# Kernel optimization log

Measured on AMD Instinct MI355X. Metric: run time of the kernel, lower is better.

The kernel has to match this reference:

```python
import jax, jax.numpy as jnp
import numpy as np

N = 6144
F_IN, H1, H2, EMB = 512, 256, 128, 64
ALPHA = 0.2  # LeakyReLU negative slope
NEG_INF = -9e15


def setup_inputs() -> dict:
    key = jax.random.key(0)
    ks = jax.random.split(key, 12)
    x = jax.random.normal(ks[0], (N, F_IN), dtype=jnp.float32)
    adj = (jax.random.uniform(ks[1], (N, N)) < 0.01).astype(jnp.float32)
    adj = jnp.maximum(adj, jnp.eye(N, dtype=jnp.float32))
    M = jax.random.uniform(ks[2], (N, N), dtype=jnp.float32)

    def glorot(k, shape):
        lim = float(np.sqrt(6.0 / (shape[0] + shape[1])))
        return jax.random.uniform(k, shape, jnp.float32, -lim, lim)

    params = {
        "W1": glorot(ks[3], (F_IN, H1)), "a_s1": glorot(ks[4], (H1, 1)), "a_n1": glorot(ks[5], (H1, 1)),
        "W2": glorot(ks[6], (H1, H2)),  "a_s2": glorot(ks[7], (H2, 1)), "a_n2": glorot(ks[8], (H2, 1)),
        "W3": glorot(ks[9], (H2, EMB)), "a_s3": glorot(ks[10], (EMB, 1)), "a_n3": glorot(ks[11], (EMB, 1)),
    }
    return {"x": x, "adj": adj, "M": M, **params}


def _gat_layer(x, adj, M, W, a_s, a_n):
    h = x @ W                                   # [N, d_out]
    e = (h @ a_s) + (h @ a_n).T                 # [N, N] pairwise logits
    e = jax.nn.leaky_relu(e * M, ALPHA)
    e = jnp.where(adj > 0, e, NEG_INF)
    att = jax.nn.softmax(e, axis=1)             # masked row softmax
    return jax.nn.elu(att @ h)


def reference(x, adj, M, W1, a_s1, a_n1, W2, a_s2, a_n2, W3, a_s3, a_n3):
    h = _gat_layer(x, adj, M, W1, a_s1, a_n1)
    h = _gat_layer(h, adj, M, W2, a_s2, a_n2)
    h = _gat_layer(h, adj, M, W3, a_s3, a_n3)
    z = h / jnp.maximum(jnp.linalg.norm(h, axis=1, keepdims=True), 1e-12)
    A_pred = jax.nn.sigmoid(z @ z.T)
    return (A_pred, z)
```

## Files before the change

### kernel.cpp

```cpp
#include <hip/hip_runtime.h>
#include <hip/hip_bf16.h>
#include <math.h>

#define NROW 6144
#define LRELU_ALPHA 0.2f
#define MAXD 128

typedef __attribute__((ext_vector_type(8))) __bf16 bf16x8;
typedef __attribute__((ext_vector_type(16))) float f32x16;

__global__ __launch_bounds__(256) void prep_all(
    const float* __restrict__ adj, const float* __restrict__ Mm,
    int* __restrict__ cnt, int* __restrict__ cidx, float* __restrict__ cmval,
    const float* __restrict__ W1, const float* __restrict__ W2, const float* __restrict__ W3,
    __bf16* __restrict__ w1h, __bf16* __restrict__ w1l,
    __bf16* __restrict__ w2h, __bf16* __restrict__ w2l,
    __bf16* __restrict__ w3h, __bf16* __restrict__ w3l,
    const float* __restrict__ as1, const float* __restrict__ an1,
    const float* __restrict__ as2, const float* __restrict__ an2,
    const float* __restrict__ as3, const float* __restrict__ an3,
    float* __restrict__ wsa1, float* __restrict__ wna1,
    float* __restrict__ wsa2, float* __restrict__ wna2,
    float* __restrict__ wsa3, float* __restrict__ wna3) {
  int b = blockIdx.x;
  if (b < NROW) {
    const int row = b;
    const int wv = threadIdx.x >> 6, lane = threadIdx.x & 63;
    __shared__ int wcnt[4];
    __shared__ int js[MAXD];
    const float4* arow = (const float4*)(adj + (size_t)row * NROW);
    const float* mrow = Mm + (size_t)row * NROW;
    float4 a[6];
#pragma unroll
    for (int it = 0; it < 6; ++it) a[it] = arow[wv * 384 + it * 64 + lane];
    int pc = 0;
#pragma unroll
    for (int it = 0; it < 6; ++it)
      pc += (a[it].x > 0.f) + (a[it].y > 0.f) + (a[it].z > 0.f) + (a[it].w > 0.f);
#pragma unroll
    for (int off = 32; off; off >>= 1) pc += __shfl_xor(pc, off);
    if (lane == 0) wcnt[wv] = pc;
    __syncthreads();
    int base = 0;
    for (int w = 0; w < wv; ++w) base += wcnt[w];
    const int total = min(wcnt[0] + wcnt[1] + wcnt[2] + wcnt[3], MAXD);
    const unsigned long long lmask = (1ull << lane) - 1ull;
#pragma unroll
    for (int it = 0; it < 6; ++it) {
      const int j = wv * 1536 + it * 256 + lane * 4;
      unsigned long long m;
      m = __ballot(a[it].x > 0.f);
      if (a[it].x > 0.f) { int p = base + __popcll(m & lmask); if (p < MAXD) js[p] = j; }
      base += __popcll(m);
      m = __ballot(a[it].y > 0.f);
      if (a[it].y > 0.f) { int p = base + __popcll(m & lmask); if (p < MAXD) js[p] = j + 1; }
      base += __popcll(m);
      m = __ballot(a[it].z > 0.f);
      if (a[it].z > 0.f) { int p = base + __popcll(m & lmask); if (p < MAXD) js[p] = j + 2; }
      base += __popcll(m);
      m = __ballot(a[it].w > 0.f);
      if (a[it].w > 0.f) { int p = base + __popcll(m & lmask); if (p < MAXD) js[p] = j + 3; }
      base += __popcll(m);
    }
    __syncthreads();
    for (int k = threadIdx.x; k < total; k += 256) {
      int j = js[k];
      cidx[(size_t)row * MAXD + k] = j;
      cmval[(size_t)row * MAXD + k] = mrow[j];
    }
    if (threadIdx.x == 0) cnt[row] = total;
    return;
  }
  b -= NROW;
  if (b < 672) {
    int idx = b * 256 + threadIdx.x;
    const float* W; __bf16 *wh, *wl; int K, D;
    if (idx < 131072) { W = W1; wh = w1h; wl = w1l; K = 512; D = 256; }
    else if (idx < 163840) { idx -= 131072; W = W2; wh = w2h; wl = w2l; K = 256; D = 128; }
    else { idx -= 163840; if (idx >= 8192) return; W = W3; wh = w3h; wl = w3l; K = 128; D = 64; }
    int k = idx / D, d = idx - k * D;
    float v = W[idx];
    __bf16 h = (__bf16)v;
    wh[(size_t)d * K + k] = h;
    wl[(size_t)d * K + k] = (__bf16)(v - (float)h);
    return;
  }
  b -= 672;
  int t = b * 256 + threadIdx.x;
  if (t < 512) {
    float s = 0.f, n = 0.f;
    for (int d = 0; d < 256; ++d) { float w = W1[t * 256 + d]; s = fmaf(w, as1[d], s); n = fmaf(w, an1[d], n); }
    wsa1[t] = s; wna1[t] = n;
  } else if (t < 768) {
    int k = t - 512;
    float s = 0.f, n = 0.f;
    for (int d = 0; d < 128; ++d) { float w = W2[k * 128 + d]; s = fmaf(w, as2[d], s); n = fmaf(w, an2[d], n); }
    wsa2[k] = s; wna2[k] = n;
  } else if (t < 896) {
    int k = t - 768;
    float s = 0.f, n = 0.f;
    for (int d = 0; d < 64; ++d) { float w = W3[k * 64 + d]; s = fmaf(w, as3[d], s); n = fmaf(w, an3[d], n); }
    wsa3[k] = s; wna3[k] = n;
  }
}

__global__ __launch_bounds__(256) void gemm_mfma(const float* __restrict__ A,
                                                 const __bf16* __restrict__ Bth,
                                                 const __bf16* __restrict__ Btl,
                                                 const float* __restrict__ wsa,
                                                 const float* __restrict__ wna,
                                                 float* __restrict__ sv,
                                                 float* __restrict__ nv,
                                                 float* __restrict__ C,
                                                 __bf16* __restrict__ Cb, int K, int D) {
  const int wv = threadIdx.x >> 6, lane = threadIdx.x & 63;
  const int l31 = lane & 31, lh = lane >> 5;
  const int ib = blockIdx.x * 64 + (wv >> 1) * 32;
  const int jb = blockIdx.y * 64 + (wv & 1) * 32;
  const float* Arow = A + (size_t)(ib + l31) * K + lh * 8;
  const __bf16* Bh = Bth + (size_t)(jb + l31) * K + lh * 8;
  const __bf16* Bl = Btl + (size_t)(jb + l31) * K + lh * 8;
  const bool do_sn = (blockIdx.y == 0) && ((wv & 1) == 0);
  f32x16 acc;
#pragma unroll
  for (int r = 0; r < 16; ++r) acc[r] = 0.f;
  float ss = 0.f, nn = 0.f;
  for (int k = 0; k < K; k += 16) {
    float4 a0 = *(const float4*)(Arow + k);
    float4 a1 = *(const float4*)(Arow + k + 4);
    bf16x8 bh = *(const bf16x8*)(Bh + k);
    bf16x8 bl = *(const bf16x8*)(Bl + k);
    float av[8] = {a0.x, a0.y, a0.z, a0.w, a1.x, a1.y, a1.z, a1.w};
    if (do_sn) {
      float4 s0 = *(const float4*)(wsa + k + lh * 8);
      float4 s1 = *(const float4*)(wsa + k + lh * 8 + 4);
      float4 n0 = *(const float4*)(wna + k + lh * 8);
      float4 n1 = *(const float4*)(wna + k + lh * 8 + 4);
      ss = fmaf(av[0], s0.x, ss); ss = fmaf(av[1], s0.y, ss);
      ss = fmaf(av[2], s0.z, ss); ss = fmaf(av[3], s0.w, ss);
      ss = fmaf(av[4], s1.x, ss); ss = fmaf(av[5], s1.y, ss);
      ss = fmaf(av[6], s1.z, ss); ss = fmaf(av[7], s1.w, ss);
      nn = fmaf(av[0], n0.x, nn); nn = fmaf(av[1], n0.y, nn);
      nn = fmaf(av[2], n0.z, nn); nn = fmaf(av[3], n0.w, nn);
      nn = fmaf(av[4], n1.x, nn); nn = fmaf(av[5], n1.y, nn);
      nn = fmaf(av[6], n1.z, nn); nn = fmaf(av[7], n1.w, nn);
    }
    bf16x8 ah, al;
#pragma unroll
    for (int t = 0; t < 8; ++t) {
      __bf16 h = (__bf16)av[t];
      ah[t] = h;
      al[t] = (__bf16)(av[t] - (float)h);
    }
    acc = __builtin_amdgcn_mfma_f32_32x32x16_bf16(ah, bh, acc, 0, 0, 0);
    acc = __builtin_amdgcn_mfma_f32_32x32x16_bf16(ah, bl, acc, 0, 0, 0);
    acc = __builtin_amdgcn_mfma_f32_32x32x16_bf16(al, bh, acc, 0, 0, 0);
  }
  if (do_sn) {
    ss += __shfl_xor(ss, 32);
    nn += __shfl_xor(nn, 32);
    if (lh == 0) { sv[ib + l31] = ss; nv[ib + l31] = nn; }
  }
#pragma unroll
  for (int r = 0; r < 16; ++r) {
    int rowi = (r & 3) + 8 * (r >> 2) + 4 * lh;
    C[(size_t)(ib + rowi) * D + jb + l31] = acc[r];
    if (Cb) Cb[(size_t)(ib + rowi) * D + jb + l31] = (__bf16)acc[r];
  }
}

template <int D, int WPR, bool BF16G, bool NORM>
__global__ __launch_bounds__(256) void attn_csr(const float* __restrict__ h,
                                                const __bf16* __restrict__ hb,
                                                const int* __restrict__ cnt,
                                                const int* __restrict__ cidx,
                                                const float* __restrict__ cmval,
                                                const float* __restrict__ sv,
                                                const float* __restrict__ nv,
                                                float* __restrict__ out,
                                                __bf16* __restrict__ zb) {
  constexpr int RPB = 4 / WPR;
  constexpr int CW = D / WPR;
  constexpr int NQ = BF16G ? 2 : CW / 64;
  __shared__ float ws[4][MAXD];
  __shared__ int js[4][MAXD];
  const int wv = threadIdx.x >> 6, lane = threadIdx.x & 63;
  const int row = blockIdx.x * RPB + wv / WPR;
  const int half = wv % WPR;
  const int c = cnt[row];
  const float si = sv[row];
  const size_t cb = (size_t)row * MAXD;

  float e0 = -1e30f, e1 = -1e30f;
  int j0 = 0, j1 = 0;
  if (lane < c) {
    j0 = cidx[cb + lane];
    float v = (si + nv[j0]) * cmval[cb + lane];
    e0 = v > 0.f ? v : LRELU_ALPHA * v;
  }
  if (lane + 64 < c) {
    j1 = cidx[cb + lane + 64];
    float v = (si + nv[j1]) * cmval[cb + lane + 64];
    e1 = v > 0.f ? v : LRELU_ALPHA * v;
  }
  float mx = fmaxf(e0, e1);
#pragma unroll
  for (int off = 32; off; off >>= 1) mx = fmaxf(mx, __shfl_xor(mx, off));
  float w0 = lane < c ? __expf(e0 - mx) : 0.f;
  float w1 = lane + 64 < c ? __expf(e1 - mx) : 0.f;
  float s = w0 + w1;
#pragma unroll
  for (int off = 32; off; off >>= 1) s += __shfl_xor(s, off);
  const float inv = 1.f / s;
  ws[wv][lane] = w0 * inv;
  ws[wv][lane + 64] = w1 * inv;
  js[wv][lane] = j0;
  js[wv][lane + 64] = j1;
  const int cbase = half * CW;
  float acc[NQ];
#pragma unroll
  for (int q = 0; q < NQ; ++q) acc[q] = 0.f;
  if (BF16G) {
#pragma unroll 8
    for (int k = 0; k < c; ++k) {
      const float wk = ws[wv][k];
      const uint32_t* hr = (const uint32_t*)(hb + (size_t)js[wv][k] * D + cbase);
      uint32_t v = hr[lane];
      acc[0] = fmaf(wk, __uint_as_float(v << 16), acc[0]);
      acc[1] = fmaf(wk, __uint_as_float(v & 0xffff0000u), acc[1]);
    }
    float2 o;
    o.x = acc[0] > 0.f ? acc[0] : expm1f(acc[0]);
    o.y = acc[1] > 0.f ? acc[1] : expm1f(acc[1]);
    *(float2*)(out + (size_t)row * D + cbase + lane * 2) = o;
  } else {
#pragma unroll 8
    for (int k = 0; k < c; ++k) {
      const float wk = ws[wv][k];
      const float* hr = h + (size_t)js[wv][k] * D + cbase;
#pragma unroll
      for (int q = 0; q < NQ; ++q) acc[q] = fmaf(wk, hr[lane + q * 64], acc[q]);
    }
    if (!NORM) {
#pragma unroll
      for (int q = 0; q < NQ; ++q) {
        float a = acc[q];
        out[(size_t)row * D + cbase + lane + q * 64] = a > 0.f ? a : expm1f(a);
      }
    } else {
      float a = acc[0];
      a = a > 0.f ? a : expm1f(a);
      float sq = a * a;
#pragma unroll
      for (int off = 32; off; off >>= 1) sq += __shfl_xor(sq, off);
      float zv = a / fmaxf(sqrtf(sq), 1e-12f);
      out[(size_t)row * 64 + lane] = zv;
      zb[(size_t)row * 64 + lane] = (__bf16)zv;
    }
  }
}

__global__ __launch_bounds__(256) void decoder_mfma(const __bf16* __restrict__ zb,
                                                    float* __restrict__ out) {
  const int wv = threadIdx.x >> 6, lane = threadIdx.x & 63;
  const int ib = blockIdx.y * 64 + (wv >> 1) * 32;
  const int jb = blockIdx.x * 64 + (wv & 1) * 32;
  const int l31 = lane & 31, lh = lane >> 5;
  const __bf16* Arow = zb + (size_t)(ib + l31) * 64 + lh * 8;
  const __bf16* Brow = zb + (size_t)(jb + l31) * 64 + lh * 8;
  f32x16 acc;
#pragma unroll
  for (int r = 0; r < 16; ++r) acc[r] = 0.f;
#pragma unroll
  for (int kk = 0; kk < 4; ++kk) {
    bf16x8 af = *(const bf16x8*)(Arow + kk * 16);
    bf16x8 bfv = *(const bf16x8*)(Brow + kk * 16);
    acc = __builtin_amdgcn_mfma_f32_32x32x16_bf16(af, bfv, acc, 0, 0, 0);
  }
#pragma unroll
  for (int r = 0; r < 16; ++r) {
    int rowi = (r & 3) + 8 * (r >> 2) + 4 * lh;
    float v = 1.f / (1.f + __expf(-acc[r]));
    out[(size_t)(ib + rowi) * NROW + jb + l31] = v;
  }
}

extern "C" void kernel_launch(void* const* d_in, const int* in_sizes, int n_in,
                              void* d_out, int out_size, void* d_ws, size_t ws_size,
                              hipStream_t stream) {
  const float* x   = (const float*)d_in[0];
  const float* adj = (const float*)d_in[1];
  const float* Mm  = (const float*)d_in[2];
  const float* W1  = (const float*)d_in[3];
  const float* as1 = (const float*)d_in[4];
  const float* an1 = (const float*)d_in[5];
  const float* W2  = (const float*)d_in[6];
  const float* as2 = (const float*)d_in[7];
  const float* an2 = (const float*)d_in[8];
  const float* W3  = (const float*)d_in[9];
  const float* as3 = (const float*)d_in[10];
  const float* an3 = (const float*)d_in[11];

  float* out = (float*)d_out;
  float* z = out + (size_t)NROW * NROW;

  float* ws = (float*)d_ws;
  float* hA   = ws;
  float* hB   = hA + (size_t)NROW * 256;
  float* sv   = hB + (size_t)NROW * 256;
  float* nv   = sv + NROW;
  float* cmv  = nv + NROW;
  int*   cix  = (int*)(cmv + (size_t)NROW * MAXD);
  int*   cct  = cix + (size_t)NROW * MAXD;
  __bf16* zb  = (__bf16*)(cct + NROW);
  __bf16* w1h = zb + (size_t)NROW * 64;
  __bf16* w1l = w1h + 512 * 256;
  __bf16* w2h = w1l + 512 * 256;
  __bf16* w2l = w2h + 256 * 128;
  __bf16* w3h = w2l + 256 * 128;
  __bf16* w3l = w3h + 128 * 64;
  float* wsa1 = (float*)(w3l + 128 * 64);
  float* wna1 = wsa1 + 512;
  float* wsa2 = wna1 + 512;
  float* wna2 = wsa2 + 256;
  float* wsa3 = wna2 + 256;
  float* wna3 = wsa3 + 128;
  __bf16* hAb = (__bf16*)(wna3 + 128);

  dim3 b256(256);

  prep_all<<<dim3(NROW + 672 + 4), b256, 0, stream>>>(
      adj, Mm, cct, cix, cmv, W1, W2, W3, w1h, w1l, w2h, w2l, w3h, w3l,
      as1, an1, as2, an2, as3, an3, wsa1, wna1, wsa2, wna2, wsa3, wna3);

  gemm_mfma<<<dim3(NROW / 64, 4), b256, 0, stream>>>(x, w1h, w1l, wsa1, wna1, sv, nv, hA, hAb, 512, 256);
  attn_csr<256, 2, true, false><<<dim3(NROW / 2), b256, 0, stream>>>(hA, hAb, cct, cix, cmv, sv, nv, hB, nullptr);

  gemm_mfma<<<dim3(NROW / 64, 2), b256, 0, stream>>>(hB, w2h, w2l, wsa2, wna2, sv, nv, hA, hAb, 256, 128);
  attn_csr<128, 1, true, false><<<dim3(NROW / 4), b256, 0, stream>>>(hA, hAb, cct, cix, cmv, sv, nv, hB, nullptr);

  gemm_mfma<<<dim3(NROW / 64, 1), b256, 0, stream>>>(hB, w3h, w3l, wsa3, wna3, sv, nv, hA, nullptr, 128, 64);
  attn_csr<64, 1, false, true><<<dim3(NROW / 4), b256, 0, stream>>>(hA, nullptr, cct, cix, cmv, sv, nv, z, zb);

  decoder_mfma<<<dim3(NROW / 64, NROW / 64), b256, 0, stream>>>(zb, out);
}
```

Before: 191.3 us.

## Fuse layer-1 GEMM with adjacency compaction and drop unused fp32 outputs

Splits the prep kernel so the weight split and projection run alone. The adjacency-to-CSR compaction is then merged with the layer-1 GEMM in one launch, so the two independent workloads overlap on the GPU. The compaction now reads the M row with coalesced float4 loads alongside adj instead of gathering M values afterwards. The fp32 GEMM outputs that the bf16-gather attention layers never read are no longer written. The risk is that attn_csr with BF16G truly never touches h, and the mixed block types in the merged kernel may balance unevenly.

```diff
diff --git a/kernel.cpp b/kernel.cpp
--- a/kernel.cpp
+++ b/kernel.cpp
@@ -9,9 +9,7 @@
 typedef __attribute__((ext_vector_type(8))) __bf16 bf16x8;
 typedef __attribute__((ext_vector_type(16))) float f32x16;
 
-__global__ __launch_bounds__(256) void prep_all(
-    const float* __restrict__ adj, const float* __restrict__ Mm,
-    int* __restrict__ cnt, int* __restrict__ cidx, float* __restrict__ cmval,
+__global__ __launch_bounds__(256) void prep_small(
     const float* __restrict__ W1, const float* __restrict__ W2, const float* __restrict__ W3,
     __bf16* __restrict__ w1h, __bf16* __restrict__ w1l,
     __bf16* __restrict__ w2h, __bf16* __restrict__ w2l,
@@ -23,55 +21,6 @@
     float* __restrict__ wsa2, float* __restrict__ wna2,
     float* __restrict__ wsa3, float* __restrict__ wna3) {
   int b = blockIdx.x;
-  if (b < NROW) {
-    const int row = b;
-    const int wv = threadIdx.x >> 6, lane = threadIdx.x & 63;
-    __shared__ int wcnt[4];
-    __shared__ int js[MAXD];
-    const float4* arow = (const float4*)(adj + (size_t)row * NROW);
-    const float* mrow = Mm + (size_t)row * NROW;
-    float4 a[6];
-#pragma unroll
-    for (int it = 0; it < 6; ++it) a[it] = arow[wv * 384 + it * 64 + lane];
-    int pc = 0;
-#pragma unroll
-    for (int it = 0; it < 6; ++it)
-      pc += (a[it].x > 0.f) + (a[it].y > 0.f) + (a[it].z > 0.f) + (a[it].w > 0.f);
-#pragma unroll
-    for (int off = 32; off; off >>= 1) pc += __shfl_xor(pc, off);
-    if (lane == 0) wcnt[wv] = pc;
-    __syncthreads();
-    int base = 0;
-    for (int w = 0; w < wv; ++w) base += wcnt[w];
-    const int total = min(wcnt[0] + wcnt[1] + wcnt[2] + wcnt[3], MAXD);
-    const unsigned long long lmask = (1ull << lane) - 1ull;
-#pragma unroll
-    for (int it = 0; it < 6; ++it) {
-      const int j = wv * 1536 + it * 256 + lane * 4;
-      unsigned long long m;
-      m = __ballot(a[it].x > 0.f);
-      if (a[it].x > 0.f) { int p = base + __popcll(m & lmask); if (p < MAXD) js[p] = j; }
-      base += __popcll(m);
-      m = __ballot(a[it].y > 0.f);
-      if (a[it].y > 0.f) { int p = base + __popcll(m & lmask); if (p < MAXD) js[p] = j + 1; }
-      base += __popcll(m);
-      m = __ballot(a[it].z > 0.f);
-      if (a[it].z > 0.f) { int p = base + __popcll(m & lmask); if (p < MAXD) js[p] = j + 2; }
-      base += __popcll(m);
-      m = __ballot(a[it].w > 0.f);
-      if (a[it].w > 0.f) { int p = base + __popcll(m & lmask); if (p < MAXD) js[p] = j + 3; }
-      base += __popcll(m);
-    }
-    __syncthreads();
-    for (int k = threadIdx.x; k < total; k += 256) {
-      int j = js[k];
-      cidx[(size_t)row * MAXD + k] = j;
-      cmval[(size_t)row * MAXD + k] = mrow[j];
-    }
-    if (threadIdx.x == 0) cnt[row] = total;
-    return;
-  }
-  b -= NROW;
   if (b < 672) {
     int idx = b * 256 + threadIdx.x;
     const float* W; __bf16 *wh, *wl; int K, D;
@@ -85,8 +34,7 @@
     wl[(size_t)d * K + k] = (__bf16)(v - (float)h);
     return;
   }
-  b -= 672;
-  int t = b * 256 + threadIdx.x;
+  int t = (b - 672) * 256 + threadIdx.x;
   if (t < 512) {
     float s = 0.f, n = 0.f;
     for (int d = 0; d < 256; ++d) { float w = W1[t * 256 + d]; s = fmaf(w, as1[d], s); n = fmaf(w, an1[d], n); }
@@ -104,23 +52,24 @@
   }
 }
 
-__global__ __launch_bounds__(256) void gemm_mfma(const float* __restrict__ A,
-                                                 const __bf16* __restrict__ Bth,
-                                                 const __bf16* __restrict__ Btl,
-                                                 const float* __restrict__ wsa,
-                                                 const float* __restrict__ wna,
-                                                 float* __restrict__ sv,
-                                                 float* __restrict__ nv,
-                                                 float* __restrict__ C,
-                                                 __bf16* __restrict__ Cb, int K, int D) {
+__device__ __forceinline__ void gemm_body(int bx, int by,
+                                          const float* __restrict__ A,
+                                          const __bf16* __restrict__ Bth,
+                                          const __bf16* __restrict__ Btl,
+                                          const float* __restrict__ wsa,
+                                          const float* __restrict__ wna,
+                                          float* __restrict__ sv,
+                                          float* __restrict__ nv,
+                                          float* __restrict__ C,
+                                          __bf16* __restrict__ Cb, int K, int D) {
   const int wv = threadIdx.x >> 6, lane = threadIdx.x & 63;
   const int l31 = lane & 31, lh = lane >> 5;
-  const int ib = blockIdx.x * 64 + (wv >> 1) * 32;
-  const int jb = blockIdx.y * 64 + (wv & 1) * 32;
+  const int ib = bx * 64 + (wv >> 1) * 32;
+  const int jb = by * 64 + (wv & 1) * 32;
   const float* Arow = A + (size_t)(ib + l31) * K + lh * 8;
   const __bf16* Bh = Bth + (size_t)(jb + l31) * K + lh * 8;
   const __bf16* Bl = Btl + (size_t)(jb + l31) * K + lh * 8;
-  const bool do_sn = (blockIdx.y == 0) && ((wv & 1) == 0);
+  const bool do_sn = (by == 0) && ((wv & 1) == 0);
   f32x16 acc;
 #pragma unroll
   for (int r = 0; r < 16; ++r) acc[r] = 0.f;
@@ -164,9 +113,82 @@
 #pragma unroll
   for (int r = 0; r < 16; ++r) {
     int rowi = (r & 3) + 8 * (r >> 2) + 4 * lh;
-    C[(size_t)(ib + rowi) * D + jb + l31] = acc[r];
+    if (C)  C[(size_t)(ib + rowi) * D + jb + l31] = acc[r];
     if (Cb) Cb[(size_t)(ib + rowi) * D + jb + l31] = (__bf16)acc[r];
   }
+}
+
+__global__ __launch_bounds__(256) void gemm_mfma(const float* __restrict__ A,
+                                                 const __bf16* __restrict__ Bth,
+                                                 const __bf16* __restrict__ Btl,
+                                                 const float* __restrict__ wsa,
+                                                 const float* __restrict__ wna,
+                                                 float* __restrict__ sv,
+                                                 float* __restrict__ nv,
+                                                 float* __restrict__ C,
+                                                 __bf16* __restrict__ Cb, int K, int D) {
+  gemm_body(blockIdx.x, blockIdx.y, A, Bth, Btl, wsa, wna, sv, nv, C, Cb, K, D);
+}
+
+__global__ __launch_bounds__(256) void mega1(
+    const float* __restrict__ adj, const float* __restrict__ Mm,
+    int* __restrict__ cnt, int* __restrict__ cidx, float* __restrict__ cmval,
+    const float* __restrict__ x,
+    const __bf16* __restrict__ w1h, const __bf16* __restrict__ w1l,
+    const float* __restrict__ wsa1, const float* __restrict__ wna1,
+    float* __restrict__ sv, float* __restrict__ nv, __bf16* __restrict__ hAb) {
+  const int b = blockIdx.x;
+  if (b < 384) {
+    gemm_body(b >> 2, b & 3, x, w1h, w1l, wsa1, wna1, sv, nv, nullptr, hAb, 512, 256);
+    return;
+  }
+  const int row = b - 384;
+  const int wv = threadIdx.x >> 6, lane = threadIdx.x & 63;
+  __shared__ int wcnt[4];
+  __shared__ int jsh[MAXD];
+  __shared__ float msh[MAXD];
+  const float4* arow = (const float4*)(adj + (size_t)row * NROW);
+  const float4* mrow = (const float4*)(Mm + (size_t)row * NROW);
+  float4 a[6], mv[6];
+#pragma unroll
+  for (int it = 0; it < 6; ++it) a[it] = arow[wv * 384 + it * 64 + lane];
+#pragma unroll
+  for (int it = 0; it < 6; ++it) mv[it] = mrow[wv * 384 + it * 64 + lane];
+  int pc = 0;
+#pragma unroll
+  for (int it = 0; it < 6; ++it)
+    pc += (a[it].x > 0.f) + (a[it].y > 0.f) + (a[it].z > 0.f) + (a[it].w > 0.f);
+#pragma unroll
+  for (int off = 32; off; off >>= 1) pc += __shfl_xor(pc, off);
+  if (lane == 0) wcnt[wv] = pc;
+  __syncthreads();
+  int base = 0;
+  for (int w = 0; w < wv; ++w) base += wcnt[w];
+  const int total = min(wcnt[0] + wcnt[1] + wcnt[2] + wcnt[3], MAXD);
+  const unsigned long long lmask = (1ull << lane) - 1ull;
+#pragma unroll
+  for (int it = 0; it < 6; ++it) {
+    const int j = wv * 1536 + it * 256 + lane * 4;
+    unsigned long long m;
+    m = __ballot(a[it].x > 0.f);
+    if (a[it].x > 0.f) { int p = base + __popcll(m & lmask); if (p < MAXD) { jsh[p] = j;     msh[p] = mv[it].x; } }
+    base += __popcll(m);
+    m = __ballot(a[it].y > 0.f);
+    if (a[it].y > 0.f) { int p = base + __popcll(m & lmask); if (p < MAXD) { jsh[p] = j + 1; msh[p] = mv[it].y; } }
+    base += __popcll(m);
+    m = __ballot(a[it].z > 0.f);
+    if (a[it].z > 0.f) { int p = base + __popcll(m & lmask); if (p < MAXD) { jsh[p] = j + 2; msh[p] = mv[it].z; } }
+    base += __popcll(m);
+    m = __ballot(a[it].w > 0.f);
+    if (a[it].w > 0.f) { int p = base + __popcll(m & lmask); if (p < MAXD) { jsh[p] = j + 3; msh[p] = mv[it].w; } }
+    base += __popcll(m);
+  }
+  __syncthreads();
+  for (int k = threadIdx.x; k < total; k += 256) {
+    cidx[(size_t)row * MAXD + k] = jsh[k];
+    cmval[(size_t)row * MAXD + k] = msh[k];
+  }
+  if (threadIdx.x == 0) cnt[row] = total;
 }
 
 template <int D, int WPR, bool BF16G, bool NORM>
@@ -329,15 +351,17 @@
 
   dim3 b256(256);
 
-  prep_all<<<dim3(NROW + 672 + 4), b256, 0, stream>>>(
-      adj, Mm, cct, cix, cmv, W1, W2, W3, w1h, w1l, w2h, w2l, w3h, w3l,
+  prep_small<<<dim3(676), b256, 0, stream>>>(
+      W1, W2, W3, w1h, w1l, w2h, w2l, w3h, w3l,
       as1, an1, as2, an2, as3, an3, wsa1, wna1, wsa2, wna2, wsa3, wna3);
 
-  gemm_mfma<<<dim3(NROW / 64, 4), b256, 0, stream>>>(x, w1h, w1l, wsa1, wna1, sv, nv, hA, hAb, 512, 256);
-  attn_csr<256, 2, true, false><<<dim3(NROW / 2), b256, 0, stream>>>(hA, hAb, cct, cix, cmv, sv, nv, hB, nullptr);
-
-  gemm_mfma<<<dim3(NROW / 64, 2), b256, 0, stream>>>(hB, w2h, w2l, wsa2, wna2, sv, nv, hA, hAb, 256, 128);
-  attn_csr<128, 1, true, false><<<dim3(NROW / 4), b256, 0, stream>>>(hA, hAb, cct, cix, cmv, sv, nv, hB, nullptr);
+  mega1<<<dim3(384 + NROW), b256, 0, stream>>>(
+      adj, Mm, cct, cix, cmv, x, w1h, w1l, wsa1, wna1, sv, nv, hAb);
+
+  attn_csr<256, 2, true, false><<<dim3(NROW / 2), b256, 0, stream>>>(nullptr, hAb, cct, cix, cmv, sv, nv, hB, nullptr);
+
+  gemm_mfma<<<dim3(NROW / 64, 2), b256, 0, stream>>>(hB, w2h, w2l, wsa2, wna2, sv, nv, nullptr, hAb, 256, 128);
+  attn_csr<128, 1, true, false><<<dim3(NROW / 4), b256, 0, stream>>>(nullptr, hAb, cct, cix, cmv, sv, nv, hB, nullptr);
 
   gemm_mfma<<<dim3(NROW / 64, 1), b256, 0, stream>>>(hB, w3h, w3l, wsa3, wna3, sv, nv, hA, nullptr, 128, 64);
   attn_csr<64, 1, false, true><<<dim3(NROW / 4), b256, 0, stream>>>(hA, nullptr, cct, cix, cmv, sv, nv, z, zb);
```

Result: slower. 201.5 us (+5.3%).
